# Performance work log

Measured on AMD Instinct MI355X. Metric: run time of the kernel, lower is better.

## Reference

```python
import jax, jax.numpy as jnp
import numpy as np

B, S, DIM = 2, 4096, 1024
H, DH = 16, 64
M = 256  # number of random features (rmfa_config['num_feats'])
EPS = 1e-6


def setup_inputs() -> dict:
    key = jax.random.key(0)
    ks = jax.random.split(key, 10)
    s_in = 1.0 / np.sqrt(DIM)
    inp = {
        "X": jax.random.normal(ks[0], (B, S, DIM), dtype=jnp.float32),
        "mask": jnp.ones((B, S), dtype=jnp.float32),
        "Wq": jax.random.normal(ks[1], (DIM, H * DH), dtype=jnp.float32) * s_in,
        "bq": jnp.zeros((H * DH,), dtype=jnp.float32),
        "Wk": jax.random.normal(ks[2], (DIM, H * DH), dtype=jnp.float32) * s_in,
        "bk": jnp.zeros((H * DH,), dtype=jnp.float32),
        "Wv": jax.random.normal(ks[3], (DIM, H * DH), dtype=jnp.float32) * s_in,
        "bv": jnp.zeros((H * DH,), dtype=jnp.float32),
        "Wf": jax.random.normal(ks[4], (H * DH, DIM), dtype=jnp.float32) * s_in,
        "bf": jnp.zeros((DIM,), dtype=jnp.float32),
        "proj": jax.random.normal(ks[5], (DH, M), dtype=jnp.float32),  # random-feature projection (frozen)
    }
    return inp


def _split_heads(x):  # [B,S,H*DH] -> [B,H,S,DH]
    return x.reshape(B, S, H, DH).transpose(0, 2, 1, 3)


def _pre_sbn(x):
    # PreSBN: project onto unit sphere (required for Schoenberg-kernel random features)
    return x / (jnp.linalg.norm(x, axis=-1, keepdims=True) + EPS)


def _phi(x, proj):
    # positive random features of the (Schoenberg/exponential) kernel on the sphere
    # x: [B,H,S,DH] unit-norm -> phi: [B,H,S,M]
    u = jnp.einsum('bhsd,dm->bhsm', x, proj)
    # ||x||^2 = 1 after pre-norm, so the -||x||^2/2 correction is a constant -0.5
    return jnp.exp(u - 0.5) / np.sqrt(M)


def reference(X, mask, Wq, bq, Wk, bk, Wv, bv, Wf, bf, proj):
    Q = _split_heads(X @ Wq + bq)
    K = _split_heads(X @ Wk + bk)
    V = _split_heads(X @ Wv + bv)
    Q = _pre_sbn(Q)
    K = _pre_sbn(K)
    # kernelized (linear) attention in fp32
    phiQ = _phi(Q.astype(jnp.float32), proj)
    phiK = _phi(K.astype(jnp.float32), proj) * mask[:, None, :, None]
    KV = jnp.einsum('bhsm,bhsd->bhmd', phiK, V.astype(jnp.float32))  # [B,H,M,DH]
    Z = phiK.sum(axis=2)                                             # [B,H,M]
    num = jnp.einsum('bhsm,bhmd->bhsd', phiQ, KV)
    den = jnp.einsum('bhsm,bhm->bhs', phiQ, Z) + EPS
    attn = num / den[..., None]
    # PostSBN(d_model=DIM//H=DH): restore scale removed by the sphere projection
    attn = attn * np.sqrt(DH)
    attn = attn.transpose(0, 2, 1, 3).reshape(B, S, H * DH)  # combine heads
    return attn @ Wf + bf
```

## Files before the change

### kernel.cpp

```cpp
#include <hip/hip_runtime.h>
#include <cmath>

typedef unsigned short u16;
typedef unsigned int   u32;
typedef __attribute__((ext_vector_type(8))) short bf16x8;
typedef __attribute__((ext_vector_type(4))) float f32x4;

#define DEV __device__ __forceinline__
#define MFMA(a,b,c) __builtin_amdgcn_mfma_f32_16x16x32_bf16((a),(b),(c),0,0,0)

#define GLOAD16(dst, src) __builtin_amdgcn_global_load_lds( \
    (const __attribute__((address_space(1))) void*)(src), \
    (__attribute__((address_space(3))) void*)(dst), 16, 0, 0)

DEV u16 f2bf(float x){ union{float f;u32 u;} v; v.f=x; u32 r=v.u+0x7FFFu+((v.u>>16)&1u); return (u16)(r>>16); }
DEV float bf2f(u16 h){ union{u32 u;float f;} v; v.u=((u32)h)<<16; return v.f; }

DEV int swz(int row, int cb){ return row*64 + ((cb ^ (row&7))*8); }

#define STGU(arr, slotsz, slot, j, P, k0) GLOAD16( \
    &(arr)[(slot)*(slotsz) + ((j)*64 + w*8)*64], \
    (P) + (size_t)((j)*64 + srow_)*1024 + (k0) + scol_)

#define GEMM_CORE_128x256(As, Bs, Ap, Bp, acc) do{ \
    const int srow_ = w*8 + (l>>3); \
    const int scol_ = ((l&7) ^ (l>>3))*8; \
    STGU(Bs,256*64,0,0,Bp,0); STGU(Bs,256*64,0,1,Bp,0); STGU(Bs,256*64,0,2,Bp,0); \
    STGU(Bs,256*64,0,3,Bp,0); STGU(As,128*64,0,0,Ap,0); STGU(As,128*64,0,1,Ap,0); \
    STGU(Bs,256*64,1,0,Bp,64); STGU(Bs,256*64,1,1,Bp,64); STGU(Bs,256*64,1,2,Bp,64); \
    STGU(Bs,256*64,1,3,Bp,64); STGU(As,128*64,1,0,Ap,64); STGU(As,128*64,1,1,Ap,64); \
    asm volatile("s_waitcnt vmcnt(6)" ::: "memory"); \
    __builtin_amdgcn_s_barrier(); \
    __builtin_amdgcn_sched_barrier(0); \
    for(int kt=0; kt<16; ++kt){ \
        const int sl = kt % 3; \
        const int st = (kt+2) % 3; \
        const int k2 = (kt+2)*64; \
        const u16* Asl = (As) + sl*(128*64); \
        const u16* Bsl = (Bs) + sl*(256*64); \
        bf16x8 bf_[4][2], af_[4][2]; \
        _Pragma("unroll") \
        for(int nt=0;nt<4;++nt) \
            _Pragma("unroll") \
            for(int ks=0;ks<2;++ks) \
                bf_[nt][ks] = *(const bf16x8*)&Bsl[swz(64*wc+16*nt+c, 4*ks+g)]; \
        _Pragma("unroll") \
        for(int mt=0;mt<4;++mt) \
            _Pragma("unroll") \
            for(int ks=0;ks<2;++ks) \
                af_[mt][ks] = *(const bf16x8*)&Asl[swz(64*wr+16*mt+c, 4*ks+g)]; \
        if (kt<=13){ STGU(Bs,256*64,st,0,Bp,k2); STGU(Bs,256*64,st,1,Bp,k2); STGU(Bs,256*64,st,2,Bp,k2); \
                     STGU(Bs,256*64,st,3,Bp,k2); STGU(As,128*64,st,0,Ap,k2); STGU(As,128*64,st,1,Ap,k2); } \
        _Pragma("unroll") \
        for(int mt=0;mt<4;++mt) \
            _Pragma("unroll") \
            for(int nt=0;nt<4;++nt) \
                _Pragma("unroll") \
                for(int ks=0;ks<2;++ks) \
                    acc[mt][nt] = MFMA(af_[mt][ks], bf_[nt][ks], acc[mt][nt]); \
        if (kt<=13)      { asm volatile("s_waitcnt vmcnt(6)" ::: "memory"); } \
        else if (kt==14) { asm volatile("s_waitcnt vmcnt(0)" ::: "memory"); } \
        __builtin_amdgcn_s_barrier(); \
        __builtin_amdgcn_sched_barrier(0); \
    } \
}while(0)

__global__ __launch_bounds__(256) void k_prep(const float* __restrict__ X,
        const float* __restrict__ Wq, const float* __restrict__ Wk,
        const float* __restrict__ Wv, const float* __restrict__ Wf,
        const float* __restrict__ proj,
        u16* __restrict__ Xb, u16* __restrict__ WT, u16* __restrict__ Wfh,
        u16* __restrict__ pPh){
    const int bid = blockIdx.x, tid = threadIdx.x;
    if (bid < 4096){
        __shared__ float t[32][33];
        const int which = bid >> 10, bb = bid & 1023;
        const float* in = (which==0) ? Wq : (which==1) ? Wk : (which==2) ? Wv : Wf;
        u16* hi = (which==3) ? Wfh : (WT + (size_t)which*1048576);
        const int r0 = (bb>>5)*32, c0 = (bb&31)*32;
        const int lr = tid>>3, lc = (tid&7)*4;
        float4 v = *(const float4*)(in + (size_t)(r0+lr)*1024 + c0 + lc);
        t[lr][lc]=v.x; t[lr][lc+1]=v.y; t[lr][lc+2]=v.z; t[lr][lc+3]=v.w;
        __syncthreads();
        ushort4 o;
        o.x=f2bf(t[lc+0][lr]); o.y=f2bf(t[lc+1][lr]);
        o.z=f2bf(t[lc+2][lr]); o.w=f2bf(t[lc+3][lr]);
        *(ushort4*)(hi + (size_t)(c0+lr)*1024 + r0+lc) = o;
    } else if (bid < 12288){
        size_t i = ((size_t)(bid-4096)*256 + tid)*4;
        float4 v = *(const float4*)(X+i);
        ushort4 o; o.x=f2bf(v.x); o.y=f2bf(v.y); o.z=f2bf(v.z); o.w=f2bf(v.w);
        *(ushort4*)(Xb+i) = o;
    } else {
        int idx = (bid-12288)*256 + tid;
        int e = idx&7, l = (idx>>3)&63, f = idx>>9;
        int nt = f>>1, ks = f&1;
        int d = 32*ks + 8*(l>>4) + e;
        int m = 16*nt + (l&15);
        pPh[idx] = f2bf(proj[d*256 + m]);
    }
}

__global__ __launch_bounds__(512,2) void k_qkv(const u16* __restrict__ Xb, const u16* __restrict__ WT,
        const float* __restrict__ bq, const float* __restrict__ bk, const float* __restrict__ bv,
        u16* __restrict__ Qb, u16* __restrict__ Kb, u16* __restrict__ VT){
    __shared__ u16 As[3*128*64];
    __shared__ u16 Bs[3*256*64];
    const int bx = blockIdx.x, y = blockIdx.y;
    const int wsel = y>>2, nb = y&3;
    const int tid = threadIdx.x, w = tid>>6, l = tid&63, g = l>>4, c = l&15;
    const int wr = w>>2, wc = w&3;
    const u16* Ap = Xb + (size_t)bx*128*1024;
    const u16* Bp = WT + (size_t)wsel*1048576 + (size_t)nb*256*1024;
    f32x4 acc[4][4];
    #pragma unroll
    for(int mt=0;mt<4;++mt)
        #pragma unroll
        for(int nt=0;nt<4;++nt) acc[mt][nt] = f32x4{0.f,0.f,0.f,0.f};

    GEMM_CORE_128x256(As, Bs, Ap, Bp, acc);

    const int n0 = nb*256 + 64*wc;
    const int b = bx>>5;
    if (wsel < 2){
        u16* Out = wsel ? Kb : Qb;
        const float* bias = wsel ? bk : bq;
        float bb[4];
        #pragma unroll
        for(int nt=0;nt<4;++nt) bb[nt] = bias[n0+16*nt+c];
        #pragma unroll
        for(int mt=0;mt<4;++mt){
            #pragma unroll
            for(int nt=0;nt<4;++nt)
                #pragma unroll
                for(int r=0;r<4;++r) acc[mt][nt][r] += bb[nt];
            #pragma unroll
            for(int r=0;r<4;++r){
                float ss = 0.f;
                #pragma unroll
                for(int nt=0;nt<4;++nt){ float vv = acc[mt][nt][r]; ss += vv*vv; }
                ss += __shfl_xor(ss,1); ss += __shfl_xor(ss,2);
                ss += __shfl_xor(ss,4); ss += __shfl_xor(ss,8);
                float sc = 1.f/(sqrtf(ss)+1e-6f);
                #pragma unroll
                for(int nt=0;nt<4;++nt) acc[mt][nt][r] *= sc;
            }
            const int rowb = bx*128 + 64*wr + 16*mt + 4*g;
            #pragma unroll
            for(int nt=0;nt<4;++nt)
                #pragma unroll
                for(int r=0;r<4;++r)
                    Out[(size_t)(rowb+r)*1024 + n0 + 16*nt + c] = f2bf(acc[mt][nt][r]);
        }
    } else {
        const int h = nb*4 + wc;
        float bb[4];
        #pragma unroll
        for(int nt=0;nt<4;++nt) bb[nt] = bv[n0+16*nt+c];
        #pragma unroll
        for(int mt=0;mt<4;++mt)
            #pragma unroll
            for(int nt=0;nt<4;++nt){
                const int d = 16*nt + c;
                const int s0m = (bx&31)*128 + 64*wr + 16*mt + 4*g;
                ushort4 o;
                o.x = f2bf(acc[mt][nt][0]+bb[nt]); o.y = f2bf(acc[mt][nt][1]+bb[nt]);
                o.z = f2bf(acc[mt][nt][2]+bb[nt]); o.w = f2bf(acc[mt][nt][3]+bb[nt]);
                *(ushort4*)(VT + ((size_t)(b*16+h)*64 + d)*4096 + s0m) = o;
            }
    }
}

__global__ __launch_bounds__(256) void k_kv(const u16* __restrict__ Kb,
        const u16* __restrict__ pPh,
        const float* __restrict__ mask, const u16* __restrict__ VT,
        float* __restrict__ KVpart, float* __restrict__ Zpart){
    __shared__ u16 phiT[256][72];
    __shared__ u16 Vs[64][72];
    __shared__ float zbuf[4][256];
    const int chunk = blockIdx.x, bh = blockIdx.y;
    const int b = bh>>4, h = bh&15;
    const int tid = threadIdx.x, wv = tid>>6, l = tid&63, g = l>>4, c = l&15;
    f32x4 kv[4][4];
    #pragma unroll
    for(int mt=0;mt<4;++mt) for(int dt=0;dt<4;++dt) kv[mt][dt] = f32x4{0.f,0.f,0.f,0.f};
    float zacc[16];
    #pragma unroll
    for(int nt=0;nt<16;++nt) zacc[nt]=0.f;
    const int vd = tid>>2, vs = (tid&3)*16;
    for(int t=0;t<4;++t){
        const int s0 = chunk*256 + t*64;
        __syncthreads();
        {
            const u16* pv = VT + ((size_t)bh*64 + vd)*4096 + s0 + vs;
            uint4 v0 = *(const uint4*)pv, v1 = *(const uint4*)(pv+8);
            *(uint4*)&Vs[vd][vs] = v0; *(uint4*)&Vs[vd][vs+8] = v1;
        }
        f32x4 ph[16];
        #pragma unroll
        for(int nt=0;nt<16;++nt) ph[nt] = f32x4{0.f,0.f,0.f,0.f};
        #pragma unroll
        for(int ks=0;ks<2;++ks){
            const int srow = s0 + 16*wv + c;
            bf16x8 ah = *(const bf16x8*)(Kb + (size_t)(b*4096+srow)*1024 + h*64 + 32*ks + 8*g);
            #pragma unroll
            for(int nt=0;nt<16;++nt){
                bf16x8 bh8 = *(const bf16x8*)(pPh + ((size_t)(nt*2+ks)*64 + l)*8);
                ph[nt] = MFMA(ah, bh8, ph[nt]);
            }
        }
        float mk[4];
        #pragma unroll
        for(int r=0;r<4;++r) mk[r] = mask[b*4096 + s0 + 16*wv + 4*g + r];
        #pragma unroll
        for(int nt=0;nt<16;++nt){
            float zs = 0.f;
            #pragma unroll
            for(int r=0;r<4;++r){
                float phv = __expf(ph[nt][r]-0.5f)*0.0625f*mk[r];
                phiT[c+16*nt][16*wv+4*g+r] = f2bf(phv);
                zs += phv;
            }
            zacc[nt] += zs;
        }
        __syncthreads();
        #pragma unroll
        for(int ks=0;ks<2;++ks){
            bf16x8 afr[4], bfr[4];
            #pragma unroll
            for(int mt=0;mt<4;++mt) afr[mt] = *(const bf16x8*)&phiT[64*wv+16*mt+c][32*ks+8*g];
            #pragma unroll
            for(int dt=0;dt<4;++dt) bfr[dt] = *(const bf16x8*)&Vs[16*dt+c][32*ks+8*g];
            #pragma unroll
            for(int mt=0;mt<4;++mt)
                #pragma unroll
                for(int dt=0;dt<4;++dt)
                    kv[mt][dt] = MFMA(afr[mt], bfr[dt], kv[mt][dt]);
        }
    }
    #pragma unroll
    for(int nt=0;nt<16;++nt){
        float z = zacc[nt];
        z += __shfl_xor(z,16); z += __shfl_xor(z,32);
        if (g==0) zbuf[wv][c+16*nt] = z;
    }
    __syncthreads();
    {
        float z = zbuf[0][tid]+zbuf[1][tid]+zbuf[2][tid]+zbuf[3][tid];
        Zpart[((size_t)bh*16+chunk)*256 + tid] = z;
    }
    float* kout = KVpart + ((size_t)bh*16+chunk)*16384;
    #pragma unroll
    for(int mt=0;mt<4;++mt)
        #pragma unroll
        for(int dt=0;dt<4;++dt)
            #pragma unroll
            for(int r=0;r<4;++r)
                kout[(64*wv+16*mt+4*g+r)*64 + 16*dt + c] = kv[mt][dt][r];
}

__global__ __launch_bounds__(256) void k_kvreduce(const float* __restrict__ KVpart,
        const float* __restrict__ Zpart, u16* __restrict__ KVT, float* __restrict__ Z){
    const int gid = blockIdx.x*256 + threadIdx.x;
    const int bh = gid >> 12;
    const int i0 = (gid & 4095) * 4;
    float4 s = {0.f,0.f,0.f,0.f};
    const float* base = KVpart + (size_t)bh*16*16384 + i0;
    #pragma unroll
    for(int ch=0; ch<16; ++ch){
        float4 v = *(const float4*)(base + (size_t)ch*16384);
        s.x+=v.x; s.y+=v.y; s.z+=v.z; s.w+=v.w;
    }
    const int m = i0 >> 6, d = i0 & 63;
    u16* dst = KVT + ((size_t)bh*64 + d)*256 + m;
    dst[0]   = f2bf(s.x);
    dst[256] = f2bf(s.y);
    dst[512] = f2bf(s.z);
    dst[768] = f2bf(s.w);
    if (gid < 8192){
        const int zbh = gid >> 8, zm = gid & 255;
        float z = 0.f;
        #pragma unroll
        for(int ch=0; ch<16; ++ch) z += Zpart[((size_t)zbh*16+ch)*256 + zm];
        Z[zbh*256 + zm] = z;
    }
}

__global__ __launch_bounds__(512) void k_attn(const u16* __restrict__ Qb,
        const u16* __restrict__ pPh,
        const u16* __restrict__ KVT, const float* __restrict__ Z, u16* __restrict__ attn){
    __shared__ u16 kvs[64*256];
    __shared__ u16 pps[16384];
    __shared__ u16 phi[128][264];
    __shared__ float Zs[256];
    const int bx = blockIdx.x, bh = blockIdx.y;
    const int b = bh>>4, h = bh&15;
    const int tid = threadIdx.x, w = tid>>6, l = tid&63, g = l>>4, c = l&15;
    if (tid < 256) Zs[tid] = Z[bh*256 + tid];
    #pragma unroll
    for(int j2=0;j2<4;++j2){
        const int base_row = (j2*8 + w)*2;
        const int row = base_row + (l>>5), cb = l&31;
        GLOAD16(kvs + base_row*256,
                KVT + (size_t)bh*16384 + row*256 + ((cb ^ (row&7))*8));
    }
    #pragma unroll
    for(int j2=0;j2<4;++j2){
        const int base = (j2*8 + w)*512;
        GLOAD16(pps + base, pPh + base + l*8);
    }
    asm volatile("s_waitcnt vmcnt(0)" ::: "memory");
    __syncthreads();

    for(int t=0;t<4;++t){
        const int s0 = bx*512 + t*128;
        f32x4 ph[16];
        #pragma unroll
        for(int nt=0;nt<16;++nt) ph[nt] = f32x4{0.f,0.f,0.f,0.f};
        #pragma unroll
        for(int ks=0;ks<2;++ks){
            const int srow = s0 + 16*w + c;
            bf16x8 ah = *(const bf16x8*)(Qb + (size_t)(b*4096+srow)*1024 + h*64 + 32*ks + 8*g);
            #pragma unroll
            for(int nt=0;nt<16;++nt){
                bf16x8 bh8 = *(const bf16x8*)(pps + ((nt*2+ks)*64 + l)*8);
                ph[nt] = MFMA(ah, bh8, ph[nt]);
            }
        }
        float den[4] = {0.f,0.f,0.f,0.f};
        #pragma unroll
        for(int nt=0;nt<16;++nt){
            float zv = Zs[c+16*nt];
            #pragma unroll
            for(int r=0;r<4;++r){
                float phv = __expf(ph[nt][r]-0.5f)*0.0625f;
                den[r] += phv*zv;
                phi[16*w+4*g+r][c+16*nt] = f2bf(phv);
            }
        }
        #pragma unroll
        for(int r=0;r<4;++r){
            den[r] += __shfl_xor(den[r],1); den[r] += __shfl_xor(den[r],2);
            den[r] += __shfl_xor(den[r],4); den[r] += __shfl_xor(den[r],8);
            den[r] += 1e-6f;
        }
        __syncthreads();
        f32x4 nm[4];
        #pragma unroll
        for(int dt=0;dt<4;++dt) nm[dt] = f32x4{0.f,0.f,0.f,0.f};
        #pragma unroll
        for(int j=0;j<8;++j){
            bf16x8 af = *(const bf16x8*)&phi[16*w+c][32*j+8*g];
            #pragma unroll
            for(int dt=0;dt<4;++dt){
                const int row = 16*dt + c, cb = 4*j + g;
                bf16x8 bfr = *(const bf16x8*)(kvs + row*256 + ((cb ^ (row&7))*8));
                nm[dt] = MFMA(af, bfr, nm[dt]);
            }
        }
        #pragma unroll
        for(int dt=0;dt<4;++dt)
            #pragma unroll
            for(int r=0;r<4;++r){
                const int srow = s0 + 16*w + 4*g + r;
                attn[(size_t)(b*4096+srow)*1024 + h*64 + 16*dt + c] = f2bf(nm[dt][r]*8.f/den[r]);
            }
        __syncthreads();
    }
}

__global__ __launch_bounds__(512,2) void k_out(const u16* __restrict__ attn,
        const u16* __restrict__ Wh, const float* __restrict__ bfb, float* __restrict__ out){
    __shared__ u16 As[3*128*64];
    __shared__ u16 Bs[3*256*64];
    const int bx = blockIdx.x, by = blockIdx.y;
    const int tid = threadIdx.x, w = tid>>6, l = tid&63, g = l>>4, c = l&15;
    const int wr = w>>2, wc = w&3;
    const u16* Ap = attn + (size_t)bx*128*1024;
    const u16* Bp = Wh + (size_t)by*256*1024;
    f32x4 acc[4][4];
    #pragma unroll
    for(int mt=0;mt<4;++mt)
        #pragma unroll
        for(int nt=0;nt<4;++nt) acc[mt][nt] = f32x4{0.f,0.f,0.f,0.f};

    GEMM_CORE_128x256(As, Bs, Ap, Bp, acc);

    const int n0 = by*256 + 64*wc;
    #pragma unroll
    for(int mt=0;mt<4;++mt){
        const int rowb = bx*128 + 64*wr + 16*mt + 4*g;
        #pragma unroll
        for(int nt=0;nt<4;++nt){
            const float bb = bfb[n0+16*nt+c];
            #pragma unroll
            for(int r=0;r<4;++r)
                out[(size_t)(rowb+r)*1024 + n0 + 16*nt + c] = acc[mt][nt][r] + bb;
        }
    }
}

extern "C" void kernel_launch(void* const* d_in, const int* in_sizes, int n_in,
                              void* d_out, int out_size, void* d_ws, size_t ws_size,
                              hipStream_t stream){
    (void)in_sizes; (void)n_in; (void)out_size;
    const float* X    = (const float*)d_in[0];
    const float* mask = (const float*)d_in[1];
    const float* Wq   = (const float*)d_in[2];
    const float* bq   = (const float*)d_in[3];
    const float* Wk   = (const float*)d_in[4];
    const float* bk   = (const float*)d_in[5];
    const float* Wv   = (const float*)d_in[6];
    const float* bv   = (const float*)d_in[7];
    const float* Wf   = (const float*)d_in[8];
    const float* bfb  = (const float*)d_in[9];
    const float* proj = (const float*)d_in[10];
    float* out = (float*)d_out;

    char* w = (char*)d_ws;
    size_t off = 0;
    auto alloc = [&](size_t n)->void*{ void* p = w + off; off = (off + n + 255) & ~(size_t)255; return p; };
    u16*   Xb     = (u16*)  alloc((size_t)8192*1024*2);
    u16*   WT     = (u16*)  alloc((size_t)3*1048576*2);
    u16*   Wfh    = (u16*)  alloc((size_t)1048576*2);
    u16*   pPh    = (u16*)  alloc(16384*2);
    u16*   Qb     = (u16*)  alloc((size_t)8192*1024*2);
    u16*   Kb     = (u16*)  alloc((size_t)8192*1024*2);
    u16*   VT     = (u16*)  alloc((size_t)32*64*4096*2);
    float* KVpart = (float*)alloc((size_t)32*16*16384*4);
    float* Zpart  = (float*)alloc((size_t)32*16*256*4);
    u16*   KVT    = (u16*)  alloc((size_t)32*64*256*2);
    float* Zr     = (float*)alloc((size_t)32*256*4);
    u16*   attnB  = (u16*)  alloc((size_t)8192*1024*2);
    if (off > ws_size) return;

    k_prep<<<dim3(12352), 256, 0, stream>>>(X, Wq, Wk, Wv, Wf, proj, Xb, WT, Wfh, pPh);
    k_qkv<<<dim3(64,12), 512, 0, stream>>>(Xb, WT, bq, bk, bv, Qb, Kb, VT);
    k_kv<<<dim3(16,32), 256, 0, stream>>>(Kb, pPh, mask, VT, KVpart, Zpart);
    k_kvreduce<<<dim3(512), 256, 0, stream>>>(KVpart, Zpart, KVT, Zr);
    k_attn<<<dim3(8,32), 512, 0, stream>>>(Qb, pPh, KVT, Zr, attnB);
    k_out<<<dim3(64,4), 512, 0, stream>>>(attnB, Wfh, bfb, out);
}
```

Before: 171.3 us.

## Double k_kv block size to 512 threads, stage projection in LDS, halve partials

The KV-accumulation kernel now runs 512 threads per block and processes 128-row sequence tiles, so each block covers 512 positions and only 8 chunks per head are produced instead of 16. The random-feature projection matrix is loaded once into shared memory with global-to-LDS loads rather than read from global memory on every MFMA step. The reduction kernel sums 8 partials instead of 16, which halves the partial-buffer traffic. In exchange the kernel launches half as many blocks (256), uses more LDS per block and adds an extra barrier per tile, which could lower occupancy and parallelism.

Result: faster. 157.5 us, median of 3 (-8.1%).

```diff
diff --git a/kernel.cpp b/kernel.cpp
--- a/kernel.cpp
+++ b/kernel.cpp
@@ -171,92 +171,102 @@
     }
 }
 
-__global__ __launch_bounds__(256) void k_kv(const u16* __restrict__ Kb,
+__global__ __launch_bounds__(512) void k_kv(const u16* __restrict__ Kb,
         const u16* __restrict__ pPh,
         const float* __restrict__ mask, const u16* __restrict__ VT,
         float* __restrict__ KVpart, float* __restrict__ Zpart){
-    __shared__ u16 phiT[256][72];
-    __shared__ u16 Vs[64][72];
-    __shared__ float zbuf[4][256];
+    __shared__ u16 pps[16384];
+    __shared__ u16 phiT[256][136];
+    __shared__ u16 Vs[64][136];
+    __shared__ float zbuf[8][256];
     const int chunk = blockIdx.x, bh = blockIdx.y;
     const int b = bh>>4, h = bh&15;
-    const int tid = threadIdx.x, wv = tid>>6, l = tid&63, g = l>>4, c = l&15;
-    f32x4 kv[4][4];
-    #pragma unroll
-    for(int mt=0;mt<4;++mt) for(int dt=0;dt<4;++dt) kv[mt][dt] = f32x4{0.f,0.f,0.f,0.f};
+    const int tid = threadIdx.x, w = tid>>6, l = tid&63, g = l>>4, c = l&15;
+    #pragma unroll
+    for(int j2=0;j2<4;++j2){
+        const int base = (j2*8 + w)*512;
+        GLOAD16(pps + base, pPh + base + l*8);
+    }
+    f32x4 kv[2][4];
+    #pragma unroll
+    for(int mt=0;mt<2;++mt) for(int dt=0;dt<4;++dt) kv[mt][dt] = f32x4{0.f,0.f,0.f,0.f};
     float zacc[16];
     #pragma unroll
     for(int nt=0;nt<16;++nt) zacc[nt]=0.f;
-    const int vd = tid>>2, vs = (tid&3)*16;
+    const int vd = tid>>3, vs8 = (tid&7)*16;
+    asm volatile("s_waitcnt vmcnt(0)" ::: "memory");
+    __syncthreads();
     for(int t=0;t<4;++t){
-        const int s0 = chunk*256 + t*64;
-        __syncthreads();
+        const int s0 = chunk*512 + t*128;
         {
-            const u16* pv = VT + ((size_t)bh*64 + vd)*4096 + s0 + vs;
+            const u16* pv = VT + ((size_t)bh*64 + vd)*4096 + s0 + vs8;
             uint4 v0 = *(const uint4*)pv, v1 = *(const uint4*)(pv+8);
-            *(uint4*)&Vs[vd][vs] = v0; *(uint4*)&Vs[vd][vs+8] = v1;
+            *(uint4*)&Vs[vd][vs8] = v0; *(uint4*)&Vs[vd][vs8+8] = v1;
         }
         f32x4 ph[16];
         #pragma unroll
         for(int nt=0;nt<16;++nt) ph[nt] = f32x4{0.f,0.f,0.f,0.f};
         #pragma unroll
         for(int ks=0;ks<2;++ks){
-            const int srow = s0 + 16*wv + c;
+            const int srow = s0 + 16*w + c;
             bf16x8 ah = *(const bf16x8*)(Kb + (size_t)(b*4096+srow)*1024 + h*64 + 32*ks + 8*g);
             #pragma unroll
             for(int nt=0;nt<16;++nt){
-                bf16x8 bh8 = *(const bf16x8*)(pPh + ((size_t)(nt*2+ks)*64 + l)*8);
+                bf16x8 bh8 = *(const bf16x8*)(pps + ((nt*2+ks)*64 + l)*8);
                 ph[nt] = MFMA(ah, bh8, ph[nt]);
             }
         }
         float mk[4];
         #pragma unroll
-        for(int r=0;r<4;++r) mk[r] = mask[b*4096 + s0 + 16*wv + 4*g + r];
+        for(int r=0;r<4;++r) mk[r] = mask[b*4096 + s0 + 16*w + 4*g + r];
         #pragma unroll
         for(int nt=0;nt<16;++nt){
             float zs = 0.f;
             #pragma unroll
             for(int r=0;r<4;++r){
                 float phv = __expf(ph[nt][r]-0.5f)*0.0625f*mk[r];
-                phiT[c+16*nt][16*wv+4*g+r] = f2bf(phv);
+                phiT[c+16*nt][16*w+4*g+r] = f2bf(phv);
                 zs += phv;
             }
             zacc[nt] += zs;
         }
         __syncthreads();
         #pragma unroll
-        for(int ks=0;ks<2;++ks){
-            bf16x8 afr[4], bfr[4];
-            #pragma unroll
-            for(int mt=0;mt<4;++mt) afr[mt] = *(const bf16x8*)&phiT[64*wv+16*mt+c][32*ks+8*g];
+        for(int ks=0;ks<4;++ks){
+            bf16x8 afr[2], bfr[4];
+            #pragma unroll
+            for(int mt=0;mt<2;++mt) afr[mt] = *(const bf16x8*)&phiT[32*w+16*mt+c][32*ks+8*g];
             #pragma unroll
             for(int dt=0;dt<4;++dt) bfr[dt] = *(const bf16x8*)&Vs[16*dt+c][32*ks+8*g];
             #pragma unroll
-            for(int mt=0;mt<4;++mt)
+            for(int mt=0;mt<2;++mt)
                 #pragma unroll
                 for(int dt=0;dt<4;++dt)
                     kv[mt][dt] = MFMA(afr[mt], bfr[dt], kv[mt][dt]);
         }
+        __syncthreads();
     }
     #pragma unroll
     for(int nt=0;nt<16;++nt){
         float z = zacc[nt];
         z += __shfl_xor(z,16); z += __shfl_xor(z,32);
-        if (g==0) zbuf[wv][c+16*nt] = z;
+        if (g==0) zbuf[w][c+16*nt] = z;
     }
     __syncthreads();
-    {
-        float z = zbuf[0][tid]+zbuf[1][tid]+zbuf[2][tid]+zbuf[3][tid];
-        Zpart[((size_t)bh*16+chunk)*256 + tid] = z;
-    }
-    float* kout = KVpart + ((size_t)bh*16+chunk)*16384;
-    #pragma unroll
-    for(int mt=0;mt<4;++mt)
+    if (tid < 256){
+        float z = 0.f;
+        #pragma unroll
+        for(int ww=0;ww<8;++ww) z += zbuf[ww][tid];
+        Zpart[((size_t)bh*8+chunk)*256 + tid] = z;
+    }
+    float* kout = KVpart + ((size_t)bh*8+chunk)*16384;
+    #pragma unroll
+    for(int mt=0;mt<2;++mt)
         #pragma unroll
         for(int dt=0;dt<4;++dt)
             #pragma unroll
             for(int r=0;r<4;++r)
-                kout[(64*wv+16*mt+4*g+r)*64 + 16*dt + c] = kv[mt][dt][r];
+                kout[(32*w+16*mt+4*g+r)*64 + 16*dt + c] = kv[mt][dt][r];
 }
 
 __global__ __launch_bounds__(256) void k_kvreduce(const float* __restrict__ KVpart,
@@ -265,9 +275,9 @@
     const int bh = gid >> 12;
     const int i0 = (gid & 4095) * 4;
     float4 s = {0.f,0.f,0.f,0.f};
-    const float* base = KVpart + (size_t)bh*16*16384 + i0;
-    #pragma unroll
-    for(int ch=0; ch<16; ++ch){
+    const float* base = KVpart + (size_t)bh*8*16384 + i0;
+    #pragma unroll
+    for(int ch=0; ch<8; ++ch){
         float4 v = *(const float4*)(base + (size_t)ch*16384);
         s.x+=v.x; s.y+=v.y; s.z+=v.z; s.w+=v.w;
     }
@@ -281,7 +291,7 @@
         const int zbh = gid >> 8, zm = gid & 255;
         float z = 0.f;
         #pragma unroll
-        for(int ch=0; ch<16; ++ch) z += Zpart[((size_t)zbh*16+ch)*256 + zm];
+        for(int ch=0; ch<8; ++ch) z += Zpart[((size_t)zbh*8+ch)*256 + zm];
         Z[zbh*256 + zm] = z;
     }
 }
@@ -427,8 +437,8 @@
     u16*   Qb     = (u16*)  alloc((size_t)8192*1024*2);
     u16*   Kb     = (u16*)  alloc((size_t)8192*1024*2);
     u16*   VT     = (u16*)  alloc((size_t)32*64*4096*2);
-    float* KVpart = (float*)alloc((size_t)32*16*16384*4);
-    float* Zpart  = (float*)alloc((size_t)32*16*256*4);
+    float* KVpart = (float*)alloc((size_t)32*8*16384*4);
+    float* Zpart  = (float*)alloc((size_t)32*8*256*4);
     u16*   KVT    = (u16*)  alloc((size_t)32*64*256*2);
     float* Zr     = (float*)alloc((size_t)32*256*4);
     u16*   attnB  = (u16*)  alloc((size_t)8192*1024*2);
@@ -436,7 +446,7 @@
 
     k_prep<<<dim3(12352), 256, 0, stream>>>(X, Wq, Wk, Wv, Wf, proj, Xb, WT, Wfh, pPh);
     k_qkv<<<dim3(64,12), 512, 0, stream>>>(Xb, WT, bq, bk, bv, Qb, Kb, VT);
-    k_kv<<<dim3(16,32), 256, 0, stream>>>(Kb, pPh, mask, VT, KVpart, Zpart);
+    k_kv<<<dim3(8,32), 512, 0, stream>>>(Kb, pPh, mask, VT, KVpart, Zpart);
     k_kvreduce<<<dim3(512), 256, 0, stream>>>(KVpart, Zpart, KVT, Zr);
     k_attn<<<dim3(8,32), 512, 0, stream>>>(Qb, pPh, KVT, Zr, attnB);
     k_out<<<dim3(64,4), 512, 0, stream>>>(attnB, Wfh, bfb, out);
```
